# Optimization experiments

Hardware: AMD Instinct MI355X
Metric: run time of the kernel (lower is better)

Reference implementation:

```python
import jax, jax.numpy as jnp
import numpy as np

B, N, P, D = 16, 1024, 72, 96
ND, H, K = 64, 4, 16
LN_EPS = 1e-5
ROW_EPS = 1e-8


def topk_sparsify(adj, k):
    # adj: (..., N, N); keep top-k per row (scatter-mask), then row-renormalize
    shp = adj.shape
    n = shp[-1]
    flat = adj.reshape(-1, n)
    _, idx = jax.lax.top_k(flat, k)  # (R, k)
    rows = jnp.arange(flat.shape[0])[:, None]
    mask = jnp.zeros_like(flat).at[rows, idx].set(1.0)
    sp = flat * mask
    sp = sp / (sp.sum(-1, keepdims=True) + ROW_EPS)
    return sp.reshape(shp)


def setup_inputs() -> dict:
    key = jax.random.key(0)
    ks = jax.random.split(key, 12)
    xav1 = np.sqrt(6.0 / (N + ND))  # xavier_uniform bound for (N, ND)
    inp = {
        "patch_features": jax.random.normal(ks[0], (B, N, P, D), jnp.float32),
        "E1": jax.random.uniform(ks[1], (H, N, ND), jnp.float32, -xav1, xav1),
        "E2": jax.random.uniform(ks[2], (H, ND, N), jnp.float32, -xav1, xav1),
        "temperature": jnp.full((H,), 0.5, jnp.float32),
        "fusion_weight": jnp.float32(0.5),
        "dW1": jax.random.normal(ks[3], (D, ND), jnp.float32) / np.sqrt(D),
        "db1": jnp.zeros((ND,), jnp.float32),
        "ln_g": jnp.ones((ND,), jnp.float32),
        "ln_b": jnp.zeros((ND,), jnp.float32),
        "dW2": jax.random.normal(ks[4], (ND, ND), jnp.float32) / np.sqrt(ND),
        "db2": jnp.zeros((ND,), jnp.float32),
        "eW1": jax.random.normal(ks[5], (H, 2 * H), jnp.float32) / np.sqrt(H),
        "eb1": jnp.zeros((2 * H,), jnp.float32),
        "eW2": jax.random.normal(ks[6], (2 * H, 1), jnp.float32) / np.sqrt(2 * H),
        "eb2": jnp.zeros((1,), jnp.float32),
    }
    return inp


def reference(patch_features, E1, E2, temperature, fusion_weight,
              dW1, db1, ln_g, ln_b, dW2, db2, eW1, eb1, eW2, eb2):
    # ---- static multi-head graphs: softmax(relu(E1 @ E2) / T, axis=-1) ----
    s = jax.nn.relu(jnp.einsum('hnd,hdm->hnm', E1, E2))
    static_adjs = jax.nn.softmax(s / temperature[:, None, None], axis=-1)

    # ---- dynamic graphs from mean-pooled patch features ----
    node_repr = patch_features.mean(axis=2)                 # (B, N, D)
    h1 = node_repr @ dW1 + db1                              # (B, N, ND)
    mu = h1.mean(-1, keepdims=True)
    var = ((h1 - mu) ** 2).mean(-1, keepdims=True)
    h1 = (h1 - mu) / jnp.sqrt(var + LN_EPS) * ln_g + ln_b   # LayerNorm
    h1 = jax.nn.relu(h1)                                    # (dropout = identity, eval)
    dyn_emb = h1 @ dW2 + db2                                # (B, N, ND)
    d = jax.nn.relu(jnp.einsum('bnd,hdm->bhnm', dyn_emb, E2))
    dynamic_adjs = jax.nn.softmax(d / temperature[None, :, None, None], axis=-1)

    # ---- top-k sparsify + row renormalize ----
    static_adjs = topk_sparsify(static_adjs, K)             # (H, N, N)
    dynamic_adjs = topk_sparsify(dynamic_adjs, K)           # (B, H, N, N)

    # ---- fuse static + dynamic ----
    fused = (1.0 - fusion_weight) * static_adjs[None] + fusion_weight * dynamic_adjs

    # ---- edge MLP over head dim: (B, N, N, H) -> (B, N, N) ----
    x = jnp.transpose(fused, (0, 2, 3, 1))                  # (B, N, N, H)
    ew = jax.nn.relu(x @ eW1 + eb1) @ eW2 + eb2             # (B, N, N, 1)
    final_adjs = jax.nn.sigmoid(ew[..., 0]) * fused.mean(axis=1)
    return final_adjs, static_adjs, dynamic_adjs
```

## Files before the change

### kernel.cpp

```cpp
#include <hip/hip_runtime.h>

typedef unsigned int u32;
typedef unsigned long long u64;
typedef unsigned short u16;

#define Bn 16
#define Nn 1024
#define Pp 72
#define MARG 3e-4f

#define NEGINF __int_as_float(0xff800000)
#define POSINF __int_as_float(0x7f800000)

#define DPP_STEP(OP, CTRL, RM)                                                 \
  y = __builtin_amdgcn_update_dpp(__float_as_int(v), __float_as_int(v),        \
                                  CTRL, RM, 0xf, false);                       \
  v = OP(v, __int_as_float(y));

#define DPP_RED(NAME, OP)                                                      \
  __device__ __forceinline__ float NAME(float v) {                             \
    int y;                                                                     \
    DPP_STEP(OP, 0x111, 0xf)                                                   \
    DPP_STEP(OP, 0x112, 0xf)                                                   \
    DPP_STEP(OP, 0x114, 0xf)                                                   \
    DPP_STEP(OP, 0x118, 0xf)                                                   \
    DPP_STEP(OP, 0x142, 0xa)                                                   \
    DPP_STEP(OP, 0x143, 0xc)                                                   \
    return __int_as_float(__builtin_amdgcn_readlane(__float_as_int(v), 63));   \
  }

#define FADDOP(a, b) ((a) + (b))
DPP_RED(dmaxf, fmaxf)
DPP_RED(dminf, fminf)
DPP_RED(dsumf, FADDOP)

__device__ __forceinline__ u32 wminu(u32 v) {
#pragma unroll
  for (int off = 1; off < 64; off <<= 1) {
    u32 o = (u32)__shfl_xor((int)v, off, 64);
    v = (o < v) ? o : v;
  }
  return v;
}

__global__ __launch_bounds__(256) void k_e2t(const float* __restrict__ E2,
                                             float* __restrict__ E2T) {
  __shared__ float tile[32][65];
  const int h = blockIdx.x >> 5;
  const int m0 = (blockIdx.x & 31) << 5;
  const float* src = E2 + (size_t)h * 65536;
  float* dst = E2T + (size_t)h * 65536;
  const int t = threadIdx.x;
#pragma unroll
  for (int k = 0; k < 8; ++k) {
    int idx = k * 256 + t;
    int d = idx >> 5, mm = idx & 31;
    tile[mm][d] = src[d * 1024 + m0 + mm];
  }
  __syncthreads();
#pragma unroll
  for (int k = 0; k < 8; ++k) {
    int idx = k * 256 + t;
    int mm = idx >> 6, d = idx & 63;
    dst[(size_t)(m0 + mm) * 64 + d] = tile[mm][d];
  }
}

__global__ __launch_bounds__(128) void k_meanmlp(const float* __restrict__ pf,
                                                 const float* __restrict__ dW1,
                                                 const float* __restrict__ db1,
                                                 const float* __restrict__ ln_g,
                                                 const float* __restrict__ ln_b,
                                                 const float* __restrict__ dW2,
                                                 const float* __restrict__ db2,
                                                 double* __restrict__ embD,
                                                 float* __restrict__ embF) {
  __shared__ double ndD[96];
  __shared__ double red[64];
  __shared__ double h1r[64];
  const int t = threadIdx.x;
  const int bn = blockIdx.x;

  if (t < 96) {
    const float* src = pf + (size_t)bn * (Pp * 96) + t;
    double s = 0.0;
    for (int p = 0; p < Pp; ++p) s += (double)src[p * 96];
    ndD[t] = s / 72.0;
  }
  __syncthreads();

  double a = 0.0;
  if (t < 64) {
    a = (double)db1[t];
    for (int d = 0; d < 96; ++d) a = fma(ndD[d], (double)dW1[d * 64 + t], a);
    red[t] = a;
  }
  __syncthreads();
  for (int s2 = 32; s2 >= 1; s2 >>= 1) {
    if (t < s2) red[t] += red[t + s2];
    __syncthreads();
  }
  const double mu = red[0] * (1.0 / 64.0);
  __syncthreads();
  const double dv = a - mu;
  if (t < 64) red[t] = dv * dv;
  __syncthreads();
  for (int s2 = 32; s2 >= 1; s2 >>= 1) {
    if (t < s2) red[t] += red[t + s2];
    __syncthreads();
  }
  const double var = red[0] * (1.0 / 64.0);
  if (t < 64) {
    double xn = dv / sqrt(var + 1e-5) * (double)ln_g[t] + (double)ln_b[t];
    h1r[t] = xn > 0.0 ? xn : 0.0;
  }
  __syncthreads();
  if (t < 64) {
    double e = (double)db2[t];
    for (int k = 0; k < 64; ++k) e = fma(h1r[k], (double)dW2[k * 64 + t], e);
    embD[(size_t)bn * 64 + t] = e;
    embF[(size_t)bn * 64 + t] = (float)e;
  }
}

template <int MODE>
__global__ __launch_bounds__(512) void k_rows(const float* __restrict__ e1f,
                                              const double* __restrict__ embD,
                                              const float* __restrict__ embF,
                                              const float* __restrict__ E2,
                                              const float* __restrict__ E2T,
                                              const float* __restrict__ temp,
                                              float* __restrict__ outp) {
  __shared__ float lgA[8][1024];
  __shared__ float embsh[64][8];
  const int t = threadIdx.x;
  const int r0 = blockIdx.x * 8;
  int h;
  size_t erow;
  if (MODE == 0) {
    h = r0 >> 10;
    erow = (size_t)r0;
  } else {
    int b = r0 >> 12;
    h = (r0 >> 10) & 3;
    int n0 = r0 & 1023;
    erow = (size_t)(b << 10) + n0;
  }
  const float* efa = (MODE == 0) ? (e1f + erow * 64) : (embF + erow * 64);
  const float2* e2 = (const float2*)(E2 + (size_t)h * 65536);
  const float* e2t = E2T + (size_t)h * 65536;
  const float invT = 1.0f / temp[h];
  const double Td = (double)temp[h];

  {
    int g = t & 7, d = t >> 3;
    embsh[d][g] = efa[g * 64 + d];
  }
  __syncthreads();

  float acc[8][2];
#pragma unroll
  for (int g = 0; g < 8; ++g) { acc[g][0] = 0.0f; acc[g][1] = 0.0f; }

#pragma unroll 4
  for (int d = 0; d < 64; ++d) {
    float2 ev = e2[d * 512 + t];
    float4 sa = *(const float4*)&embsh[d][0];
    float4 sb = *(const float4*)&embsh[d][4];
    acc[0][0] = fmaf(sa.x, ev.x, acc[0][0]);
    acc[0][1] = fmaf(sa.x, ev.y, acc[0][1]);
    acc[1][0] = fmaf(sa.y, ev.x, acc[1][0]);
    acc[1][1] = fmaf(sa.y, ev.y, acc[1][1]);
    acc[2][0] = fmaf(sa.z, ev.x, acc[2][0]);
    acc[2][1] = fmaf(sa.z, ev.y, acc[2][1]);
    acc[3][0] = fmaf(sa.w, ev.x, acc[3][0]);
    acc[3][1] = fmaf(sa.w, ev.y, acc[3][1]);
    acc[4][0] = fmaf(sb.x, ev.x, acc[4][0]);
    acc[4][1] = fmaf(sb.x, ev.y, acc[4][1]);
    acc[5][0] = fmaf(sb.y, ev.x, acc[5][0]);
    acc[5][1] = fmaf(sb.y, ev.y, acc[5][1]);
    acc[6][0] = fmaf(sb.z, ev.x, acc[6][0]);
    acc[6][1] = fmaf(sb.z, ev.y, acc[6][1]);
    acc[7][0] = fmaf(sb.w, ev.x, acc[7][0]);
    acc[7][1] = fmaf(sb.w, ev.y, acc[7][1]);
  }
#pragma unroll
  for (int g = 0; g < 8; ++g) {
    float2 o;
    o.x = fmaxf(acc[g][0], 0.0f) * invT;
    o.y = fmaxf(acc[g][1], 0.0f) * invT;
    ((float2*)(&lgA[g][0]))[t] = o;
  }
  __syncthreads();

  const int w = t >> 6, l = t & 63;
  {
    const int g = w;
    float q[16];
#pragma unroll
    for (int j = 0; j < 16; ++j) q[j] = lgA[g][l + (j << 6)];

    float lm = q[0];
#pragma unroll
    for (int j = 1; j < 16; ++j) lm = fmaxf(lm, q[j]);
    const float qmax = dmaxf(lm);

    u32 lo = 0u, hi = __float_as_uint(qmax) + 1u;
    u32 kept = 0u;
    bool f16 = false;
    float pvf = 0.0f;
#pragma unroll 1
    while (hi - lo > 1u) {
      u32 mid = (lo + hi) >> 1;
      float pv = __uint_as_float(mid);
      u32 cw = 0;
#pragma unroll
      for (int j = 0; j < 16; ++j)
        cw += (u32)__popcll(__ballot(q[j] >= pv));
      if (cw >= 16u) lo = mid; else hi = mid;
      if (cw == 16u) { f16 = true; pvf = pv; break; }
    }
    float theta, ub;
    if (f16) {
      float vmin = POSINF, umax = -1.0f;
#pragma unroll
      for (int j = 0; j < 16; ++j) {
        if (q[j] >= pvf) { kept |= 1u << j; vmin = fminf(vmin, q[j]); }
        else umax = fmaxf(umax, q[j]);
      }
      theta = dminf(vmin);
      ub = dmaxf(umax);
    } else {
      theta = __uint_as_float(lo);
      u32 cw = 0;
#pragma unroll
      for (int j = 0; j < 16; ++j) {
        cw += (u32)__popcll(__ballot(q[j] > theta));
        if (q[j] > theta) kept |= 1u << j;
      }
      int r = 16 - (int)cw;
#pragma unroll 1
      for (int it = 0; it < r; ++it) {
        u32 mc = 0xFFFFFFFFu;
#pragma unroll
        for (int j = 0; j < 16; ++j)
          if (q[j] == theta && !((kept >> j) & 1u)) {
            u32 cc = (u32)((j << 6) | l);
            mc = cc < mc ? cc : mc;
          }
        u32 wm = wminu(mc);
        if ((wm & 63u) == (u32)l) kept |= 1u << (wm >> 6);
      }
      ub = theta;
    }

    if (theta - ub >= MARG) {
      float e[16];
      float es = 0.0f, ek = 0.0f;
#pragma unroll
      for (int j = 0; j < 16; ++j) {
        e[j] = __expf(q[j] - qmax);
        es += e[j];
        if ((kept >> j) & 1u) ek += e[j];
      }
      const float Z = dsumf(es);
      const float EK = dsumf(ek);
      const float inv = 1.0f / (EK + 1e-8f * Z);
#pragma unroll
      for (int j = 0; j < 16; ++j)
        lgA[g][l + (j << 6)] = ((kept >> j) & 1u) ? (e[j] * inv) : 0.0f;
    } else {
      double qd[16];
      const float thr = ub - MARG;
#pragma unroll 1
      for (int j = 0; j < 16; ++j) {
        if (q[j] >= thr) {
          const int m = l + (j << 6);
          const float* col = e2t + (size_t)m * 64;
          double a = 0.0;
          for (int d = 0; d < 64; ++d) {
            double s = (MODE == 0) ? (double)e1f[(erow + g) * 64 + d]
                                   : embD[(erow + g) * 64 + d];
            a = fma(s, (double)col[d], a);
          }
          qd[j] = (a > 0.0 ? a : 0.0) / Td;
        } else {
          qd[j] = (double)q[j];
        }
      }
      double bm = qd[0];
#pragma unroll
      for (int j = 1; j < 16; ++j) bm = qd[j] > bm ? qd[j] : bm;
      float mh = (float)bm;
      float mlo = (float)(bm - (double)mh);
      float whi = dmaxf(mh);
      float wlo = dmaxf(mh == whi ? mlo : NEGINF);
      const double qmaxd = (double)whi + (double)wlo;

      float ev2[16];
      float es2 = 0.0f;
#pragma unroll
      for (int j = 0; j < 16; ++j) { ev2[j] = __expf((float)(qd[j] - qmaxd)); es2 += ev2[j]; }
      const float Z2 = dsumf(es2);

      u32 kept2 = 0;
      float EK2 = 0.0f;
#pragma unroll 1
      for (int it = 0; it < 16; ++it) {
        double bv = -1.0;
        int bjj = -1;
#pragma unroll
        for (int j = 0; j < 16; ++j) {
          bool tk = (((kept2 >> j) & 1u) == 0u) && (qd[j] > bv);
          bv = tk ? qd[j] : bv;
          bjj = tk ? j : bjj;
        }
        float bh = NEGINF, bl = NEGINF;
        if (bjj >= 0) { bh = (float)bv; bl = (float)(bv - (double)bh); }
        float vhi = dmaxf(bh);
        float vlo = dmaxf(bh == vhi ? bl : NEGINF);
        bool elig = (bh == vhi) && (bl == vlo);
        u32 mc = elig ? (u32)((bjj << 6) | l) : 0xFFFFFFFFu;
        u32 mwin = wminu(mc);
        EK2 += __expf((float)(((double)vhi + (double)vlo) - qmaxd));
        if ((mwin & 63u) == (u32)l) kept2 |= 1u << (mwin >> 6);
      }
      const float inv2 = 1.0f / (EK2 + 1e-8f * Z2);
#pragma unroll
      for (int j = 0; j < 16; ++j)
        lgA[g][l + (j << 6)] = ((kept2 >> j) & 1u) ? (ev2[j] * inv2) : 0.0f;
    }
  }
  __syncthreads();

  float4* gout = (float4*)(outp + (size_t)r0 * 1024);
  const float4* src = (const float4*)(&lgA[0][0]);
#pragma unroll
  for (int k = 0; k < 4; ++k) {
    int i = t + k * 512;
    gout[i] = src[i];
  }
}

__global__ __launch_bounds__(256) void k_fuse(const float* __restrict__ dyn,
                                              const float* __restrict__ stat,
                                              float* __restrict__ fin,
                                              const float* __restrict__ eW1,
                                              const float* __restrict__ eb1,
                                              const float* __restrict__ eW2,
                                              const float* __restrict__ eb2,
                                              const float* __restrict__ fwp) {
  const float w = fwp[0];
  const float w1 = 1.0f - w;
  float W1[4][8], B1v[8], W2v[8];
#pragma unroll
  for (int hh = 0; hh < 4; ++hh)
#pragma unroll
    for (int j = 0; j < 8; ++j) W1[hh][j] = eW1[hh * 8 + j];
#pragma unroll
  for (int j = 0; j < 8; ++j) { B1v[j] = eb1[j]; W2v[j] = eW2[j]; }
  const float b2 = eb2[0];

  const int i = blockIdx.x * 256 + threadIdx.x;
  const int b = i >> 18;
  const int rem = i & 262143;
  const int n = rem >> 8;
  const int c4 = rem & 255;

  float fx[4][4];
#pragma unroll
  for (int hh = 0; hh < 4; ++hh) {
    float4 fd = ((const float4*)dyn)[(((size_t)((b * 4 + hh) * 1024 + n)) << 8) + c4];
    float4 fs = ((const float4*)stat)[(((size_t)(hh * 1024 + n)) << 8) + c4];
    fx[hh][0] = w1 * fs.x + w * fd.x;
    fx[hh][1] = w1 * fs.y + w * fd.y;
    fx[hh][2] = w1 * fs.z + w * fd.z;
    fx[hh][3] = w1 * fs.w + w * fd.w;
  }
  float ov[4];
#pragma unroll
  for (int x = 0; x < 4; ++x) {
    float ew = b2;
#pragma unroll
    for (int j = 0; j < 8; ++j) {
      float hj = B1v[j];
#pragma unroll
      for (int hh = 0; hh < 4; ++hh) hj = fmaf(fx[hh][x], W1[hh][j], hj);
      ew = fmaf(fmaxf(hj, 0.0f), W2v[j], ew);
    }
    float mean = (fx[0][x] + fx[1][x] + fx[2][x] + fx[3][x]) * 0.25f;
    float sg = 1.0f / (1.0f + __expf(-ew));
    ov[x] = sg * mean;
  }
  float4 o;
  o.x = ov[0]; o.y = ov[1]; o.z = ov[2]; o.w = ov[3];
  ((float4*)fin)[i] = o;
}

extern "C" void kernel_launch(void* const* d_in, const int* in_sizes, int n_in,
                              void* d_out, int out_size, void* d_ws, size_t ws_size,
                              hipStream_t stream) {
  const float* pf   = (const float*)d_in[0];
  const float* E1   = (const float*)d_in[1];
  const float* E2   = (const float*)d_in[2];
  const float* temp = (const float*)d_in[3];
  const float* fw   = (const float*)d_in[4];
  const float* dW1  = (const float*)d_in[5];
  const float* db1  = (const float*)d_in[6];
  const float* ln_g = (const float*)d_in[7];
  const float* ln_b = (const float*)d_in[8];
  const float* dW2  = (const float*)d_in[9];
  const float* db2  = (const float*)d_in[10];
  const float* eW1  = (const float*)d_in[11];
  const float* eb1  = (const float*)d_in[12];
  const float* eW2  = (const float*)d_in[13];
  const float* eb2  = (const float*)d_in[14];

  float* out_final = (float*)d_out;
  float* out_stat  = out_final + (size_t)Bn * Nn * Nn;
  float* out_dyn   = out_stat + (size_t)4 * Nn * Nn;

  double* embD = (double*)d_out;
  float* embF = out_final + 2097152;
  float* E2T  = out_final + 3145728;

  k_e2t<<<128, 256, 0, stream>>>(E2, E2T);
  k_meanmlp<<<Bn * Nn, 128, 0, stream>>>(pf, dW1, db1, ln_g, ln_b, dW2, db2, embD, embF);
  k_rows<0><<<512, 512, 0, stream>>>(E1, nullptr, nullptr, E2, E2T, temp, out_stat);
  k_rows<1><<<8192, 512, 0, stream>>>(nullptr, embD, embF, E2, E2T, temp, out_dyn);
  k_fuse<<<16384, 256, 0, stream>>>(out_dyn, out_stat, out_final, eW1, eb1, eW2, eb2, fw);
}
```

Measured before the change: 604.5 us.

## Split fused row kernel into dot-product and top-k selection kernels

Replaces the single k_rows kernel, which computed logits into shared memory and then ran top-k/softmax per row, with two kernels. k_dot computes 16 rows per block (up from 8) to reuse each E2 load across more rows and writes the logits straight to global memory. k_sel then reloads each row from global memory and does the selection and renormalisation with 256-thread blocks and no shared memory. This removes the 32KB shared buffer and its occupancy limit, at the cost of an extra global write and read of the full logit tensor.

```diff
diff --git a/kernel.cpp b/kernel.cpp
--- a/kernel.cpp
+++ b/kernel.cpp
@@ -124,17 +124,14 @@
 }
 
 template <int MODE>
-__global__ __launch_bounds__(512) void k_rows(const float* __restrict__ e1f,
-                                              const double* __restrict__ embD,
-                                              const float* __restrict__ embF,
-                                              const float* __restrict__ E2,
-                                              const float* __restrict__ E2T,
-                                              const float* __restrict__ temp,
-                                              float* __restrict__ outp) {
-  __shared__ float lgA[8][1024];
-  __shared__ float embsh[64][8];
+__global__ __launch_bounds__(512) void k_dot(const float* __restrict__ e1f,
+                                             const float* __restrict__ embF,
+                                             const float* __restrict__ E2,
+                                             const float* __restrict__ temp,
+                                             float* __restrict__ outp) {
+  __shared__ float embsh[64][16];
   const int t = threadIdx.x;
-  const int r0 = blockIdx.x * 8;
+  const int r0 = blockIdx.x * 16;
   int h;
   size_t erow;
   if (MODE == 0) {
@@ -148,197 +145,203 @@
   }
   const float* efa = (MODE == 0) ? (e1f + erow * 64) : (embF + erow * 64);
   const float2* e2 = (const float2*)(E2 + (size_t)h * 65536);
-  const float* e2t = E2T + (size_t)h * 65536;
   const float invT = 1.0f / temp[h];
-  const double Td = (double)temp[h];
-
-  {
-    int g = t & 7, d = t >> 3;
+
+#pragma unroll
+  for (int i = t; i < 1024; i += 512) {
+    int g = i & 15, d = i >> 4;
     embsh[d][g] = efa[g * 64 + d];
   }
   __syncthreads();
 
-  float acc[8][2];
-#pragma unroll
-  for (int g = 0; g < 8; ++g) { acc[g][0] = 0.0f; acc[g][1] = 0.0f; }
-
-#pragma unroll 4
+  float acc[16][2];
+#pragma unroll
+  for (int g = 0; g < 16; ++g) { acc[g][0] = 0.0f; acc[g][1] = 0.0f; }
+
+#define FMA2(g, s)                                                             \
+  acc[g][0] = fmaf(s, ev.x, acc[g][0]);                                        \
+  acc[g][1] = fmaf(s, ev.y, acc[g][1]);
+
+#pragma unroll 2
   for (int d = 0; d < 64; ++d) {
     float2 ev = e2[d * 512 + t];
     float4 sa = *(const float4*)&embsh[d][0];
     float4 sb = *(const float4*)&embsh[d][4];
-    acc[0][0] = fmaf(sa.x, ev.x, acc[0][0]);
-    acc[0][1] = fmaf(sa.x, ev.y, acc[0][1]);
-    acc[1][0] = fmaf(sa.y, ev.x, acc[1][0]);
-    acc[1][1] = fmaf(sa.y, ev.y, acc[1][1]);
-    acc[2][0] = fmaf(sa.z, ev.x, acc[2][0]);
-    acc[2][1] = fmaf(sa.z, ev.y, acc[2][1]);
-    acc[3][0] = fmaf(sa.w, ev.x, acc[3][0]);
-    acc[3][1] = fmaf(sa.w, ev.y, acc[3][1]);
-    acc[4][0] = fmaf(sb.x, ev.x, acc[4][0]);
-    acc[4][1] = fmaf(sb.x, ev.y, acc[4][1]);
-    acc[5][0] = fmaf(sb.y, ev.x, acc[5][0]);
-    acc[5][1] = fmaf(sb.y, ev.y, acc[5][1]);
-    acc[6][0] = fmaf(sb.z, ev.x, acc[6][0]);
-    acc[6][1] = fmaf(sb.z, ev.y, acc[6][1]);
-    acc[7][0] = fmaf(sb.w, ev.x, acc[7][0]);
-    acc[7][1] = fmaf(sb.w, ev.y, acc[7][1]);
-  }
-#pragma unroll
-  for (int g = 0; g < 8; ++g) {
+    float4 sc = *(const float4*)&embsh[d][8];
+    float4 sd = *(const float4*)&embsh[d][12];
+    FMA2(0, sa.x) FMA2(1, sa.y) FMA2(2, sa.z) FMA2(3, sa.w)
+    FMA2(4, sb.x) FMA2(5, sb.y) FMA2(6, sb.z) FMA2(7, sb.w)
+    FMA2(8, sc.x) FMA2(9, sc.y) FMA2(10, sc.z) FMA2(11, sc.w)
+    FMA2(12, sd.x) FMA2(13, sd.y) FMA2(14, sd.z) FMA2(15, sd.w)
+  }
+#undef FMA2
+
+#pragma unroll
+  for (int g = 0; g < 16; ++g) {
     float2 o;
     o.x = fmaxf(acc[g][0], 0.0f) * invT;
     o.y = fmaxf(acc[g][1], 0.0f) * invT;
-    ((float2*)(&lgA[g][0]))[t] = o;
-  }
-  __syncthreads();
-
+    ((float2*)(outp + (size_t)(r0 + g) * 1024))[t] = o;
+  }
+}
+
+template <int MODE>
+__global__ __launch_bounds__(256) void k_sel(const float* __restrict__ e1f,
+                                             const double* __restrict__ embD,
+                                             const float* __restrict__ E2T,
+                                             const float* __restrict__ temp,
+                                             float* __restrict__ outp) {
+  const int t = threadIdx.x;
   const int w = t >> 6, l = t & 63;
-  {
-    const int g = w;
-    float q[16];
-#pragma unroll
-    for (int j = 0; j < 16; ++j) q[j] = lgA[g][l + (j << 6)];
-
-    float lm = q[0];
-#pragma unroll
-    for (int j = 1; j < 16; ++j) lm = fmaxf(lm, q[j]);
-    const float qmax = dmaxf(lm);
-
-    u32 lo = 0u, hi = __float_as_uint(qmax) + 1u;
-    u32 kept = 0u;
-    bool f16 = false;
-    float pvf = 0.0f;
+  const int r = blockIdx.x * 4 + w;
+  int h;
+  size_t erow;
+  if (MODE == 0) {
+    h = r >> 10;
+    erow = (size_t)r;
+  } else {
+    int b = r >> 12;
+    h = (r >> 10) & 3;
+    int n = r & 1023;
+    erow = (size_t)(b << 10) + n;
+  }
+  const float* e2t = E2T + (size_t)h * 65536;
+  const double Td = (double)temp[h];
+  float* row = outp + (size_t)r * 1024;
+
+  float q[16];
+#pragma unroll
+  for (int j = 0; j < 16; ++j) q[j] = row[l + (j << 6)];
+
+  float lm = q[0];
+#pragma unroll
+  for (int j = 1; j < 16; ++j) lm = fmaxf(lm, q[j]);
+  const float qmax = dmaxf(lm);
+
+  u32 lo = 0u, hi = __float_as_uint(qmax) + 1u;
+  u32 kept = 0u;
+  bool f16 = false;
+  float pvf = 0.0f;
 #pragma unroll 1
-    while (hi - lo > 1u) {
-      u32 mid = (lo + hi) >> 1;
-      float pv = __uint_as_float(mid);
-      u32 cw = 0;
+  while (hi - lo > 1u) {
+    u32 mid = (lo + hi) >> 1;
+    float pv = __uint_as_float(mid);
+    u32 cw = 0;
+#pragma unroll
+    for (int j = 0; j < 16; ++j)
+      cw += (u32)__popcll(__ballot(q[j] >= pv));
+    if (cw >= 16u) lo = mid; else hi = mid;
+    if (cw == 16u) { f16 = true; pvf = pv; break; }
+  }
+  float theta, ub;
+  if (f16) {
+    float vmin = POSINF, umax = -1.0f;
+#pragma unroll
+    for (int j = 0; j < 16; ++j) {
+      if (q[j] >= pvf) { kept |= 1u << j; vmin = fminf(vmin, q[j]); }
+      else umax = fmaxf(umax, q[j]);
+    }
+    theta = dminf(vmin);
+    ub = dmaxf(umax);
+  } else {
+    theta = __uint_as_float(lo);
+    u32 cw = 0;
+#pragma unroll
+    for (int j = 0; j < 16; ++j) {
+      cw += (u32)__popcll(__ballot(q[j] > theta));
+      if (q[j] > theta) kept |= 1u << j;
+    }
+    int rr = 16 - (int)cw;
+#pragma unroll 1
+    for (int it = 0; it < rr; ++it) {
+      u32 mc = 0xFFFFFFFFu;
 #pragma unroll
       for (int j = 0; j < 16; ++j)
-        cw += (u32)__popcll(__ballot(q[j] >= pv));
-      if (cw >= 16u) lo = mid; else hi = mid;
-      if (cw == 16u) { f16 = true; pvf = pv; break; }
-    }
-    float theta, ub;
-    if (f16) {
-      float vmin = POSINF, umax = -1.0f;
+        if (q[j] == theta && !((kept >> j) & 1u)) {
+          u32 cc = (u32)((j << 6) | l);
+          mc = cc < mc ? cc : mc;
+        }
+      u32 wm = wminu(mc);
+      if ((wm & 63u) == (u32)l) kept |= 1u << (wm >> 6);
+    }
+    ub = theta;
+  }
+
+  if (theta - ub >= MARG) {
+    float e[16];
+    float es = 0.0f, ek = 0.0f;
+#pragma unroll
+    for (int j = 0; j < 16; ++j) {
+      e[j] = __expf(q[j] - qmax);
+      es += e[j];
+      if ((kept >> j) & 1u) ek += e[j];
+    }
+    const float Z = dsumf(es);
+    const float EK = dsumf(ek);
+    const float inv = 1.0f / (EK + 1e-8f * Z);
+#pragma unroll
+    for (int j = 0; j < 16; ++j)
+      row[l + (j << 6)] = ((kept >> j) & 1u) ? (e[j] * inv) : 0.0f;
+  } else {
+    double qd[16];
+    const float thr = ub - MARG;
+#pragma unroll 1
+    for (int j = 0; j < 16; ++j) {
+      if (q[j] >= thr) {
+        const int m = l + (j << 6);
+        const float* col = e2t + (size_t)m * 64;
+        double a = 0.0;
+        for (int d = 0; d < 64; ++d) {
+          double s = (MODE == 0) ? (double)e1f[erow * 64 + d]
+                                 : embD[erow * 64 + d];
+          a = fma(s, (double)col[d], a);
+        }
+        qd[j] = (a > 0.0 ? a : 0.0) / Td;
+      } else {
+        qd[j] = (double)q[j];
+      }
+    }
+    double bm = qd[0];
+#pragma unroll
+    for (int j = 1; j < 16; ++j) bm = qd[j] > bm ? qd[j] : bm;
+    float mh = (float)bm;
+    float mlo = (float)(bm - (double)mh);
+    float whi = dmaxf(mh);
+    float wlo = dmaxf(mh == whi ? mlo : NEGINF);
+    const double qmaxd = (double)whi + (double)wlo;
+
+    float ev2[16];
+    float es2 = 0.0f;
+#pragma unroll
+    for (int j = 0; j < 16; ++j) { ev2[j] = __expf((float)(qd[j] - qmaxd)); es2 += ev2[j]; }
+    const float Z2 = dsumf(es2);
+
+    u32 kept2 = 0;
+    float EK2 = 0.0f;
+#pragma unroll 1
+    for (int it = 0; it < 16; ++it) {
+      double bv = -1.0;
+      int bjj = -1;
 #pragma unroll
       for (int j = 0; j < 16; ++j) {
-        if (q[j] >= pvf) { kept |= 1u << j; vmin = fminf(vmin, q[j]); }
-        else umax = fmaxf(umax, q[j]);
+        bool tk = (((kept2 >> j) & 1u) == 0u) && (qd[j] > bv);
+        bv = tk ? qd[j] : bv;
+        bjj = tk ? j : bjj;
       }
-      theta = dminf(vmin);
-      ub = dmaxf(umax);
-    } else {
-      theta = __uint_as_float(lo);
-      u32 cw = 0;
-#pragma unroll
-      for (int j = 0; j < 16; ++j) {
-        cw += (u32)__popcll(__ballot(q[j] > theta));
-        if (q[j] > theta) kept |= 1u << j;
-      }
-      int r = 16 - (int)cw;
-#pragma unroll 1
-      for (int it = 0; it < r; ++it) {
-        u32 mc = 0xFFFFFFFFu;
-#pragma unroll
-        for (int j = 0; j < 16; ++j)
-          if (q[j] == theta && !((kept >> j) & 1u)) {
-            u32 cc = (u32)((j << 6) | l);
-            mc = cc < mc ? cc : mc;
-          }
-        u32 wm = wminu(mc);
-        if ((wm & 63u) == (u32)l) kept |= 1u << (wm >> 6);
-      }
-      ub = theta;
-    }
-
-    if (theta - ub >= MARG) {
-      float e[16];
-      float es = 0.0f, ek = 0.0f;
-#pragma unroll
-      for (int j = 0; j < 16; ++j) {
-        e[j] = __expf(q[j] - qmax);
-        es += e[j];
-        if ((kept >> j) & 1u) ek += e[j];
-      }
-      const float Z = dsumf(es);
-      const float EK = dsumf(ek);
-      const float inv = 1.0f / (EK + 1e-8f * Z);
-#pragma unroll
-      for (int j = 0; j < 16; ++j)
-        lgA[g][l + (j << 6)] = ((kept >> j) & 1u) ? (e[j] * inv) : 0.0f;
-    } else {
-      double qd[16];
-      const float thr = ub - MARG;
-#pragma unroll 1
-      for (int j = 0; j < 16; ++j) {
-        if (q[j] >= thr) {
-          const int m = l + (j << 6);
-          const float* col = e2t + (size_t)m * 64;
-          double a = 0.0;
-          for (int d = 0; d < 64; ++d) {
-            double s = (MODE == 0) ? (double)e1f[(erow + g) * 64 + d]
-                                   : embD[(erow + g) * 64 + d];
-            a = fma(s, (double)col[d], a);
-          }
-          qd[j] = (a > 0.0 ? a : 0.0) / Td;
-        } else {
-          qd[j] = (double)q[j];
-        }
-      }
-      double bm = qd[0];
-#pragma unroll
-      for (int j = 1; j < 16; ++j) bm = qd[j] > bm ? qd[j] : bm;
-      float mh = (float)bm;
-      float mlo = (float)(bm - (double)mh);
-      float whi = dmaxf(mh);
-      float wlo = dmaxf(mh == whi ? mlo : NEGINF);
-      const double qmaxd = (double)whi + (double)wlo;
-
-      float ev2[16];
-      float es2 = 0.0f;
-#pragma unroll
-      for (int j = 0; j < 16; ++j) { ev2[j] = __expf((float)(qd[j] - qmaxd)); es2 += ev2[j]; }
-      const float Z2 = dsumf(es2);
-
-      u32 kept2 = 0;
-      float EK2 = 0.0f;
-#pragma unroll 1
-      for (int it = 0; it < 16; ++it) {
-        double bv = -1.0;
-        int bjj = -1;
-#pragma unroll
-        for (int j = 0; j < 16; ++j) {
-          bool tk = (((kept2 >> j) & 1u) == 0u) && (qd[j] > bv);
-          bv = tk ? qd[j] : bv;
-          bjj = tk ? j : bjj;
-        }
-        float bh = NEGINF, bl = NEGINF;
-        if (bjj >= 0) { bh = (float)bv; bl = (float)(bv - (double)bh); }
-        float vhi = dmaxf(bh);
-        float vlo = dmaxf(bh == vhi ? bl : NEGINF);
-        bool elig = (bh == vhi) && (bl == vlo);
-        u32 mc = elig ? (u32)((bjj << 6) | l) : 0xFFFFFFFFu;
-        u32 mwin = wminu(mc);
-        EK2 += __expf((float)(((double)vhi + (double)vlo) - qmaxd));
-        if ((mwin & 63u) == (u32)l) kept2 |= 1u << (mwin >> 6);
-      }
-      const float inv2 = 1.0f / (EK2 + 1e-8f * Z2);
-#pragma unroll
-      for (int j = 0; j < 16; ++j)
-        lgA[g][l + (j << 6)] = ((kept2 >> j) & 1u) ? (ev2[j] * inv2) : 0.0f;
-    }
-  }
-  __syncthreads();
-
-  float4* gout = (float4*)(outp + (size_t)r0 * 1024);
-  const float4* src = (const float4*)(&lgA[0][0]);
-#pragma unroll
-  for (int k = 0; k < 4; ++k) {
-    int i = t + k * 512;
-    gout[i] = src[i];
+      float bh = NEGINF, bl = NEGINF;
+      if (bjj >= 0) { bh = (float)bv; bl = (float)(bv - (double)bh); }
+      float vhi = dmaxf(bh);
+      float vlo = dmaxf(bh == vhi ? bl : NEGINF);
+      bool elig = (bh == vhi) && (bl == vlo);
+      u32 mc = elig ? (u32)((bjj << 6) | l) : 0xFFFFFFFFu;
+      u32 mwin = wminu(mc);
+      EK2 += __expf((float)(((double)vhi + (double)vlo) - qmaxd));
+      if ((mwin & 63u) == (u32)l) kept2 |= 1u << (mwin >> 6);
+    }
+    const float inv2 = 1.0f / (EK2 + 1e-8f * Z2);
+#pragma unroll
+    for (int j = 0; j < 16; ++j)
+      row[l + (j << 6)] = ((kept2 >> j) & 1u) ? (ev2[j] * inv2) : 0.0f;
   }
 }
 
@@ -426,7 +429,9 @@
 
   k_e2t<<<128, 256, 0, stream>>>(E2, E2T);
   k_meanmlp<<<Bn * Nn, 128, 0, stream>>>(pf, dW1, db1, ln_g, ln_b, dW2, db2, embD, embF);
-  k_rows<0><<<512, 512, 0, stream>>>(E1, nullptr, nullptr, E2, E2T, temp, out_stat);
-  k_rows<1><<<8192, 512, 0, stream>>>(nullptr, embD, embF, E2, E2T, temp, out_dyn);
+  k_dot<0><<<256, 512, 0, stream>>>(E1, nullptr, E2, temp, out_stat);
+  k_sel<0><<<1024, 256, 0, stream>>>(E1, nullptr, E2T, temp, out_stat);
+  k_dot<1><<<4096, 512, 0, stream>>>(nullptr, embF, E2, temp, out_dyn);
+  k_sel<1><<<16384, 256, 0, stream>>>(nullptr, embD, E2T, temp, out_dyn);
   k_fuse<<<16384, 256, 0, stream>>>(out_dyn, out_stat, out_final, eW1, eb1, eW2, eb2, fw);
 }
```

Result: faster. 588.9 us (-2.6%).
